# Performance work log

Hardware: AMD Instinct MI355X
Metric: run time of the kernel (lower is better)

## Reference

```python
import jax, jax.numpy as jnp
import numpy as np

B, T, H, W = 32, 100, 16, 16
CIN, HID, COUT, K = 64, 128, 64, 5
EPS = 1e-3      # keras LayerNormalization default epsilon
ALPHA = 0.2     # LeakyReLU slope


def _conv_same(x, w):
    # x: [B,H,W,Cin], w: [kh,kw,Cin,Cout] -> [B,H,W,Cout], SAME padding, stride 1
    return jax.lax.conv_general_dilated(
        x, w, window_strides=(1, 1), padding='SAME',
        dimension_numbers=('NHWC', 'HWIO', 'NHWC'))


def setup_inputs() -> dict:
    key = jax.random.key(0)
    ks = jax.random.split(key, 8)
    s = 0.05
    return {
        'initial_input': jax.random.normal(ks[0], (B, 1, H, W, CIN), jnp.float32),
        'h0': jax.random.normal(ks[1], (B, H, W, HID), jnp.float32) * s,
        'c0': jax.random.normal(ks[2], (B, H, W, HID), jnp.float32) * s,
        'targets': jax.random.normal(ks[3], (B, T, H, W, CIN), jnp.float32),
        'autoreg_prob': jnp.float32(0.5),
        # ConvLSTM2D params (keras gate order: i, f, c, o stacked on last axis)
        'Wx': jax.random.normal(ks[4], (K, K, CIN, 4 * HID), jnp.float32) * s,
        'Wh': jax.random.normal(ks[5], (K, K, HID, 4 * HID), jnp.float32) * s,
        'b': jnp.zeros((4 * HID,), jnp.float32),
        # Conv2D(64, 3, same)
        'conv_w': jax.random.normal(ks[6], (3, 3, HID, COUT), jnp.float32) * s,
        'conv_b': jnp.zeros((COUT,), jnp.float32),
        # LayerNorm (axis=-1)
        'gamma': jnp.ones((COUT,), jnp.float32),
        'beta': jnp.zeros((COUT,), jnp.float32),
    }


def reference(initial_input, h0, c0, targets, autoreg_prob,
              Wx, Wh, b, conv_w, conv_b, gamma, beta):
    T_ = targets.shape[1]
    t_switch = jnp.float32(T_) * autoreg_prob
    x0 = initial_input[:, 0]                       # [B,H,W,CIN] (seq-len-1 ConvLSTM step)
    tgt_t = jnp.transpose(targets, (1, 0, 2, 3, 4))  # [T,B,H,W,CIN]
    ts = jnp.arange(T_)

    def step(carry, inp):
        x, h, c = carry
        t, tgt = inp
        # ConvLSTM2D cell (one timestep)
        g = _conv_same(x, Wx) + _conv_same(h, Wh) + b   # [B,H,W,4*HID]
        i_g, f_g, c_g, o_g = jnp.split(g, 4, axis=-1)
        c = jax.nn.sigmoid(f_g) * c + jax.nn.sigmoid(i_g) * jnp.tanh(c_g)
        h = jax.nn.sigmoid(o_g) * jnp.tanh(c)
        # Conv2D -> LayerNorm(axis=-1) -> LeakyReLU(0.2)
        y = _conv_same(h, conv_w) + conv_b              # [B,H,W,COUT]
        mu = jnp.mean(y, axis=-1, keepdims=True)
        var = jnp.var(y, axis=-1, keepdims=True)
        y = (y - mu) * jax.lax.rsqrt(var + EPS) * gamma + beta
        out = jnp.where(y >= 0, y, ALPHA * y)
        # autoreg phase feeds output back; teacher phase feeds targets[:, t]
        next_x = jnp.where(t.astype(jnp.float32) < t_switch, out, tgt)
        return (next_x, h, c), out

    _, outs = jax.lax.scan(step, (x0, h0, c0), (ts, tgt_t))
    return jnp.transpose(outs, (1, 0, 2, 3, 4))        # [B,T,H,W,COUT]
```

## Files before the change

### kernel.cpp

```cpp
#include <hip/hip_runtime.h>

#define TT   100
#define PADW 20
#define HID  128
#define CIN  64
#define COUT 64
#define ALPHA 0.2f
#define LNEPS 1e-3f

typedef _Float16 f16;
typedef __attribute__((ext_vector_type(8))) _Float16 f16x8;
typedef __attribute__((ext_vector_type(4))) float f32x4;

__device__ __forceinline__ float fsig(float x) {
  return __builtin_amdgcn_rcpf(1.f + __builtin_amdgcn_exp2f(-1.44269504089f * x));
}
__device__ __forceinline__ float ftanh(float x) {
  return 1.f - 2.f * __builtin_amdgcn_rcpf(1.f + __builtin_amdgcn_exp2f(2.88539008178f * x));
}
__device__ __forceinline__ void gload16(const void* g, void* l) {
  __builtin_amdgcn_global_load_lds((const __attribute__((address_space(1))) void*)g,
                                   (__attribute__((address_space(3))) void*)l,
                                   16, 0, 0);
}

__global__ __launch_bounds__(512, 1) void kA6(
    const f16* __restrict__ Xh, const f16* __restrict__ Xl,
    const f16* __restrict__ Hch, const f16* __restrict__ Hcl,
    f16* __restrict__ Hnh, f16* __restrict__ Hnl,
    const f16* __restrict__ Wch, const f16* __restrict__ Wcl,
    const float* __restrict__ bp, float* __restrict__ cst) {
  __shared__ __align__(16) char smem[131072];
  f16 (*sAh)[128][64] = (f16(*)[128][64])(smem);
  f16 (*sAl)[128][64] = (f16(*)[128][64])(smem + 32768);
  f16 (*sBh)[128][64] = (f16(*)[128][64])(smem + 65536);
  f16 (*sBl)[128][64] = (f16(*)[128][64])(smem + 98304);
  float* macc = (float*)smem;

  const int tid = threadIdx.x;
  const int l = tid & 63, w = tid >> 6;
  const int h = w & 1, q = w >> 1;
  const int qm = q >> 1, qn = q & 1;
  const int xcd = blockIdx.x & 7, slot = blockIdx.x >> 3;
  const int ni = xcd >> 1;
  const int mi = ((xcd & 1) << 5) + slot;
  const int cof = ((l & 7) ^ (l >> 3)) * 8;

  int posA[2], wBo[2];
#pragma unroll
  for (int i = 0; i < 2; ++i) {
    const int r = w * 16 + i * 8 + (l >> 3);
    const int m = mi * 128 + r;
    const int b = m >> 8, y = (m >> 4) & 15, x = m & 15;
    posA[i] = (b * PADW + y + 2) * PADW + (x + 2);
    wBo[i] = (ni * 128 + r) * 192 + cof;
  }

  auto stage = [&](int bf, int it) {
    const int tap = it / 3, sub = it - tap * 3;
    const int dy = tap / 5, dx = tap - dy * 5;
    const int dt = (dy - 2) * PADW + (dx - 2);
    if (sub == 0) {
#pragma unroll
      for (int i = 0; i < 2; ++i) {
        gload16(Xh + (posA[i] + dt) * CIN + cof, &sAh[bf][w * 16 + i * 8][0]);
        gload16(Xl + (posA[i] + dt) * CIN + cof, &sAl[bf][w * 16 + i * 8][0]);
      }
    } else {
      const int ho = (sub - 1) * 64 + cof;
#pragma unroll
      for (int i = 0; i < 2; ++i) {
        gload16(Hch + (posA[i] + dt) * HID + ho, &sAh[bf][w * 16 + i * 8][0]);
        gload16(Hcl + (posA[i] + dt) * HID + ho, &sAl[bf][w * 16 + i * 8][0]);
      }
    }
    const int wo = tap * (512 * 192) + sub * 64;
#pragma unroll
    for (int i = 0; i < 2; ++i) {
      gload16(Wch + wBo[i] + wo, &sBh[bf][w * 16 + i * 8][0]);
      gload16(Wcl + wBo[i] + wo, &sBl[bf][w * 16 + i * 8][0]);
    }
  };

  f32x4 acc[4][4] = {};

  stage(0, 0);
  __syncthreads();

  const int co = ((h * 4 + (l >> 4)) ^ (l & 7)) * 8;

  int buf = 0;
  for (int it = 0; it < 75; ++it) {
    if (it < 74) stage(buf ^ 1, it + 1);
    f16x8 avh[4], avl[4], bvh[4], bvl[4];
#pragma unroll
    for (int fm = 0; fm < 4; ++fm) {
      avh[fm] = *(const f16x8*)&sAh[buf][qm * 64 + fm * 16 + (l & 15)][co];
      avl[fm] = *(const f16x8*)&sAl[buf][qm * 64 + fm * 16 + (l & 15)][co];
    }
#pragma unroll
    for (int fn = 0; fn < 4; ++fn) {
      bvh[fn] = *(const f16x8*)&sBh[buf][qn * 64 + fn * 16 + (l & 15)][co];
      bvl[fn] = *(const f16x8*)&sBl[buf][qn * 64 + fn * 16 + (l & 15)][co];
    }
#pragma unroll
    for (int fm = 0; fm < 4; ++fm)
#pragma unroll
      for (int fn = 0; fn < 4; ++fn) {
        acc[fm][fn] =
            __builtin_amdgcn_mfma_f32_16x16x32_f16(avh[fm], bvh[fn], acc[fm][fn], 0, 0, 0);
        acc[fm][fn] =
            __builtin_amdgcn_mfma_f32_16x16x32_f16(avl[fm], bvh[fn], acc[fm][fn], 0, 0, 0);
        acc[fm][fn] =
            __builtin_amdgcn_mfma_f32_16x16x32_f16(avh[fm], bvl[fn], acc[fm][fn], 0, 0, 0);
      }
    __syncthreads();
    buf ^= 1;
  }

  if (h == 1) {
#pragma unroll
    for (int fm = 0; fm < 4; ++fm)
#pragma unroll
      for (int fn = 0; fn < 4; ++fn)
#pragma unroll
        for (int j = 0; j < 4; ++j)
          macc[q * 4096 + ((fm * 4 + fn) * 4 + j) * 64 + l] = acc[fm][fn][j];
  }
  __syncthreads();
  if (h == 0) {
#pragma unroll
    for (int fm = 0; fm < 4; ++fm)
#pragma unroll
      for (int fn = 0; fn < 4; ++fn)
#pragma unroll
        for (int j = 0; j < 4; ++j)
          acc[fm][fn][j] += macc[q * 4096 + ((fm * 4 + fn) * 4 + j) * 64 + l];

#pragma unroll
    for (int fn = 0; fn < 4; ++fn) {
      const int col = ni * 128 + qn * 64 + fn * 16 + (l & 15);
      const float bias = bp[col];
      const int ch = col >> 2;
#pragma unroll
      for (int fm = 0; fm < 4; ++fm) {
#pragma unroll
        for (int j = 0; j < 4; ++j) {
          const float v = acc[fm][fn][j] + bias;
          const float t1 = __shfl_xor(v, 1);
          const float t2 = __shfl_xor(v, 2);
          const float t3 = __shfl_xor(t1, 2);
          if ((l & 3) == 0) {
            const int m = mi * 128 + qm * 64 + fm * 16 + ((l >> 4) << 2) + j;
            const int cidx = m * HID + ch;
            const float cold = cst[cidx];
            const float cn = fsig(t1) * cold + fsig(v) * ftanh(t2);
            cst[cidx] = cn;
            const float hh_ = fsig(t3) * ftanh(cn);
            const int b = m >> 8, y = (m >> 4) & 15, x = m & 15;
            const int pidx = ((b * PADW + y + 2) * PADW + (x + 2)) * HID + ch;
            const f16 hv = (f16)hh_;
            Hnh[pidx] = hv;
            Hnl[pidx] = (f16)(hh_ - (float)hv);
          }
        }
      }
    }
  }
}

__global__ __launch_bounds__(256, 2) void kB(
    const f16* __restrict__ Hnh, const f16* __restrict__ Hnl,
    const f16* __restrict__ Cwh, const f16* __restrict__ Cwl,
    const float* __restrict__ cb, const float* __restrict__ gam,
    const float* __restrict__ bet, const float* __restrict__ tgt,
    const float* __restrict__ prob, float* __restrict__ outp,
    f16* __restrict__ Xph, f16* __restrict__ Xpl, int t) {
  __shared__ __align__(16) f16 sAh[2][32][64];
  __shared__ __align__(16) f16 sAl[2][32][64];
  __shared__ __align__(16) f16 sBh[2][64][64];
  __shared__ __align__(16) f16 sBl[2][64][64];
  __shared__ __align__(16) float yl[32][68];
  const int tid = threadIdx.x;
  const int l = tid & 63, w = tid >> 6;
  const int wm = w >> 1, wn = w & 1;
  const int mi = blockIdx.x;
  const int cof = ((l & 7) ^ (l >> 3)) * 8;

  const int rA = w * 8 + (l >> 3);
  const int mA = mi * 32 + rA;
  const int bA = mA >> 8, yA = (mA >> 4) & 15, xA = mA & 15;
  const int posA = (bA * PADW + yA + 2) * PADW + (xA + 2);
  int wBo[2];
#pragma unroll
  for (int i = 0; i < 2; ++i) wBo[i] = (w * 16 + i * 8 + (l >> 3)) * HID + cof;

  auto stage = [&](int bf, int it) {
    const int tap = it >> 1, sub = it & 1;
    const int dy = tap / 3, dx = tap - dy * 3;
    const int dt = (dy - 1) * PADW + (dx - 1);
    gload16(Hnh + (posA + dt) * HID + sub * 64 + cof, &sAh[bf][w * 8][0]);
    gload16(Hnl + (posA + dt) * HID + sub * 64 + cof, &sAl[bf][w * 8][0]);
    const int wo = tap * (64 * HID) + sub * 64;
#pragma unroll
    for (int i = 0; i < 2; ++i) {
      gload16(Cwh + wBo[i] + wo, &sBh[bf][w * 16 + i * 8][0]);
      gload16(Cwl + wBo[i] + wo, &sBl[bf][w * 16 + i * 8][0]);
    }
  };

  f32x4 acc[2] = {};

  stage(0, 0);
  __syncthreads();

  int buf = 0;
  for (int it = 0; it < 18; ++it) {
    if (it < 17) stage(buf ^ 1, it + 1);
#pragma unroll
    for (int kk = 0; kk < 2; ++kk) {
      const int co = ((kk * 4 + (l >> 4)) ^ (l & 7)) * 8;
      const f16x8 ah = *(const f16x8*)&sAh[buf][wm * 16 + (l & 15)][co];
      const f16x8 al = *(const f16x8*)&sAl[buf][wm * 16 + (l & 15)][co];
#pragma unroll
      for (int fn = 0; fn < 2; ++fn) {
        const f16x8 bh = *(const f16x8*)&sBh[buf][wn * 32 + fn * 16 + (l & 15)][co];
        const f16x8 bl = *(const f16x8*)&sBl[buf][wn * 32 + fn * 16 + (l & 15)][co];
        acc[fn] = __builtin_amdgcn_mfma_f32_16x16x32_f16(ah, bh, acc[fn], 0, 0, 0);
        acc[fn] = __builtin_amdgcn_mfma_f32_16x16x32_f16(al, bh, acc[fn], 0, 0, 0);
        acc[fn] = __builtin_amdgcn_mfma_f32_16x16x32_f16(ah, bl, acc[fn], 0, 0, 0);
      }
    }
    __syncthreads();
    buf ^= 1;
  }

#pragma unroll
  for (int fn = 0; fn < 2; ++fn) {
    const int col = wn * 32 + fn * 16 + (l & 15);
    const float bias = cb[col];
#pragma unroll
    for (int j = 0; j < 4; ++j) yl[wm * 16 + (l >> 4) * 4 + j][col] = acc[fn][j] + bias;
  }
  __syncthreads();

  if (tid < 128) {
    const int row = tid >> 2, part = tid & 3;
    f32x4 vv[4];
    float s = 0.f, q = 0.f;
#pragma unroll
    for (int k2 = 0; k2 < 4; ++k2) {
      vv[k2] = *(const f32x4*)&yl[row][part * 16 + k2 * 4];
#pragma unroll
      for (int e = 0; e < 4; ++e) { const float f = vv[k2][e]; s += f; q += f * f; }
    }
    s += __shfl_xor(s, 1); q += __shfl_xor(q, 1);
    s += __shfl_xor(s, 2); q += __shfl_xor(q, 2);
    const float mean = s * 0.015625f;
    const float var = q * 0.015625f - mean * mean;
    const float rs = __builtin_amdgcn_rsqf(fmaxf(var, 0.f) + LNEPS);
    const int m = mi * 32 + row;
    const int b = m >> 8, pos = m & 255;
    const int py = pos >> 4, px = pos & 15;
    const long obase = (((long)b * TT + t) * 256 + pos) * COUT + part * 16;
    float* op = outp + obase;
    const float* tp = tgt + obase;
    const bool ar = (float)t < 100.f * prob[0];
    const int xoff = ((b * PADW + py + 2) * PADW + px + 2) * CIN + part * 16;
    f16x8 ph[2], pl[2];
#pragma unroll
    for (int k2 = 0; k2 < 4; ++k2) {
      f32x4 o4;
#pragma unroll
      for (int e = 0; e < 4; ++e) {
        const int c = part * 16 + k2 * 4 + e;
        float val = (vv[k2][e] - mean) * rs * gam[c] + bet[c];
        val = val >= 0.f ? val : ALPHA * val;
        o4[e] = val;
        const float nxt = ar ? val : tp[k2 * 4 + e];
        const f16 nh = (f16)nxt;
        const int i16 = k2 * 4 + e;
        ph[i16 >> 3][i16 & 7] = nh;
        pl[i16 >> 3][i16 & 7] = (f16)(nxt - (float)nh);
      }
      *(f32x4*)(op + k2 * 4) = o4;
    }
    *(f16x8*)(Xph + xoff) = ph[0];
    *(f16x8*)(Xph + xoff + 8) = ph[1];
    *(f16x8*)(Xpl + xoff) = pl[0];
    *(f16x8*)(Xpl + xoff + 8) = pl[1];
  }
}

__global__ void k_wcomb(const float* __restrict__ Wx, const float* __restrict__ Wh,
                        f16* __restrict__ Wch, f16* __restrict__ Wcl) {
  const int idx = blockIdx.x * 256 + threadIdx.x;
  if (idx >= 25 * 512 * 192) return;
  const int c = idx % 192, r = idx / 192;
  const int n = r % 512, tap = r / 512;
  const int ch = n >> 2, g = n & 3, no = g * 128 + ch;
  const float v = (c < 64) ? Wx[(tap * 64 + c) * 512 + no]
                           : Wh[(tap * 128 + (c - 64)) * 512 + no];
  const f16 vh = (f16)v;
  Wch[idx] = vh;
  Wcl[idx] = (f16)(v - (float)vh);
}
__global__ void k_wconv(const float* __restrict__ cw, f16* __restrict__ Cwh,
                        f16* __restrict__ Cwl) {
  const int idx = blockIdx.x * 256 + threadIdx.x;
  if (idx >= 9 * 64 * 128) return;
  const int c = idx % 128, r = idx / 128;
  const int n = r % 64, tap = r / 64;
  const float v = cw[(tap * 128 + c) * 64 + n];
  const f16 vh = (f16)v;
  Cwh[idx] = vh;
  Cwl[idx] = (f16)(v - (float)vh);
}
__global__ void k_bperm(const float* __restrict__ b, float* __restrict__ bp) {
  const int n = blockIdx.x * 256 + threadIdx.x;
  if (n < 512) bp[n] = b[(n & 3) * 128 + (n >> 2)];
}
__global__ void k_init(const float* __restrict__ x0, const float* __restrict__ h0,
                       const float* __restrict__ c0, f16* __restrict__ Xph,
                       f16* __restrict__ Xpl, f16* __restrict__ Hh, f16* __restrict__ Hl,
                       float* __restrict__ cst) {
  const int idx = blockIdx.x * 256 + threadIdx.x;
  if (idx < 32 * 256 * 64) {
    const int ch = idx & 63, m = idx >> 6;
    const int b = m >> 8, y = (m >> 4) & 15, x = m & 15;
    const int p = ((b * PADW + y + 2) * PADW + x + 2) * CIN + ch;
    const float v = x0[idx];
    const f16 vh = (f16)v;
    Xph[p] = vh;
    Xpl[p] = (f16)(v - (float)vh);
  } else if (idx < 32 * 256 * 64 + 32 * 256 * 128) {
    const int j = idx - 32 * 256 * 64;
    const int ch = j & 127, m = j >> 7;
    const int b = m >> 8, y = (m >> 4) & 15, x = m & 15;
    const int p = ((b * PADW + y + 2) * PADW + x + 2) * HID + ch;
    const float v = h0[j];
    const f16 vh = (f16)v;
    Hh[p] = vh;
    Hl[p] = (f16)(v - (float)vh);
  } else if (idx < 32 * 256 * 64 + 2 * 32 * 256 * 128) {
    const int j = idx - 32 * 256 * 64 - 32 * 256 * 128;
    cst[j] = c0[j];
  }
}

extern "C" void kernel_launch(void* const* d_in, const int* in_sizes, int n_in,
                              void* d_out, int out_size, void* d_ws, size_t ws_size,
                              hipStream_t stream) {
  (void)in_sizes; (void)n_in; (void)out_size; (void)ws_size;
  const float* x0  = (const float*)d_in[0];
  const float* h0  = (const float*)d_in[1];
  const float* c0  = (const float*)d_in[2];
  const float* tgt = (const float*)d_in[3];
  const float* pr  = (const float*)d_in[4];
  const float* Wx  = (const float*)d_in[5];
  const float* Wh  = (const float*)d_in[6];
  const float* bb  = (const float*)d_in[7];
  const float* cw  = (const float*)d_in[8];
  const float* cbv = (const float*)d_in[9];
  const float* gam = (const float*)d_in[10];
  const float* bet = (const float*)d_in[11];
  float* outp = (float*)d_out;
  char* ws = (char*)d_ws;
  f16*   Xph = (f16*)(ws + 0);
  f16*   Xpl = (f16*)(ws + 1638400);
  f16*   Hh0 = (f16*)(ws + 3276800);
  f16*   Hl0 = (f16*)(ws + 6553600);
  f16*   Hh1 = (f16*)(ws + 9830400);
  f16*   Hl1 = (f16*)(ws + 13107200);
  float* cst = (float*)(ws + 16384000);
  f16*   Wch = (f16*)(ws + 20578304);
  f16*   Wcl = (f16*)(ws + 25493504);
  f16*   Cwh = (f16*)(ws + 30408704);
  f16*   Cwl = (f16*)(ws + 30556160);
  float* bp  = (float*)(ws + 30703616);

  hipMemsetAsync(Xph, 0, 1638400, stream);
  hipMemsetAsync(Xpl, 0, 1638400, stream);
  hipMemsetAsync(Hh0, 0, 3276800, stream);
  hipMemsetAsync(Hl0, 0, 3276800, stream);
  hipMemsetAsync(Hh1, 0, 3276800, stream);
  hipMemsetAsync(Hl1, 0, 3276800, stream);
  k_wcomb<<<9600, 256, 0, stream>>>(Wx, Wh, Wch, Wcl);
  k_wconv<<<288, 256, 0, stream>>>(cw, Cwh, Cwl);
  k_bperm<<<2, 256, 0, stream>>>(bb, bp);
  k_init<<<10240, 256, 0, stream>>>(x0, h0, c0, Xph, Xpl, Hh0, Hl0, cst);

  for (int t = 0; t < TT; ++t) {
    f16* hch = (t & 1) ? Hh1 : Hh0;
    f16* hcl = (t & 1) ? Hl1 : Hl0;
    f16* hnh = (t & 1) ? Hh0 : Hh1;
    f16* hnl = (t & 1) ? Hl0 : Hl1;
    kA6<<<256, 512, 0, stream>>>(Xph, Xpl, hch, hcl, hnh, hnl, Wch, Wcl, bp, cst);
    kB<<<256, 256, 0, stream>>>(hnh, hnl, Cwh, Cwl, cbv, gam, bet, tgt, pr, outp, Xph, Xpl, t);
  }
}
```

Baseline: 13.81 ms.

## Triple-buffer activation tiles and prefetch two stages ahead in ConvLSTM GEMM

The gate-convolution kernel now splits staging into separate activation and weight loads. Activations are triple-buffered and fetched two iterations ahead, while weights stay double-buffered one ahead. A full __syncthreads is replaced by a partial vmcnt wait plus a raw barrier, so the next loads can stay in flight across iterations, and MFMA issue priority is raised with s_setprio. This uses 160KB of LDS and depends on hand-counted vmcnt values, which would be wrong if the compiler issued the loads in a different number or order. The tail iterations redundantly reload stage 74.

```diff
diff --git a/kernel.cpp b/kernel.cpp
--- a/kernel.cpp
+++ b/kernel.cpp
@@ -24,17 +24,17 @@
                                    16, 0, 0);
 }
 
-__global__ __launch_bounds__(512, 1) void kA6(
+__global__ __launch_bounds__(512, 1) void kA7(
     const f16* __restrict__ Xh, const f16* __restrict__ Xl,
     const f16* __restrict__ Hch, const f16* __restrict__ Hcl,
     f16* __restrict__ Hnh, f16* __restrict__ Hnl,
     const f16* __restrict__ Wch, const f16* __restrict__ Wcl,
     const float* __restrict__ bp, float* __restrict__ cst) {
-  __shared__ __align__(16) char smem[131072];
+  __shared__ __align__(16) char smem[163840];
   f16 (*sAh)[128][64] = (f16(*)[128][64])(smem);
-  f16 (*sAl)[128][64] = (f16(*)[128][64])(smem + 32768);
-  f16 (*sBh)[128][64] = (f16(*)[128][64])(smem + 65536);
-  f16 (*sBl)[128][64] = (f16(*)[128][64])(smem + 98304);
+  f16 (*sAl)[128][64] = (f16(*)[128][64])(smem + 49152);
+  f16 (*sBh)[128][64] = (f16(*)[128][64])(smem + 98304);
+  f16 (*sBl)[128][64] = (f16(*)[128][64])(smem + 131072);
   float* macc = (float*)smem;
 
   const int tid = threadIdx.x;
@@ -56,7 +56,7 @@
     wBo[i] = (ni * 128 + r) * 192 + cof;
   }
 
-  auto stage = [&](int bf, int it) {
+  auto stageA = [&](int bf, int it) {
     const int tap = it / 3, sub = it - tap * 3;
     const int dy = tap / 5, dx = tap - dy * 5;
     const int dt = (dy - 2) * PADW + (dx - 2);
@@ -74,6 +74,9 @@
         gload16(Hcl + (posA[i] + dt) * HID + ho, &sAl[bf][w * 16 + i * 8][0]);
       }
     }
+  };
+  auto stageB = [&](int bf, int it) {
+    const int tap = it / 3, sub = it - tap * 3;
     const int wo = tap * (512 * 192) + sub * 64;
 #pragma unroll
     for (int i = 0; i < 2; ++i) {
@@ -84,25 +87,33 @@
 
   f32x4 acc[4][4] = {};
 
-  stage(0, 0);
-  __syncthreads();
+  stageA(0, 0);
+  stageB(0, 0);
+  stageA(1, 1);
+  asm volatile("s_waitcnt vmcnt(4)" ::: "memory");
+  __builtin_amdgcn_s_barrier();
 
   const int co = ((h * 4 + (l >> 4)) ^ (l & 7)) * 8;
 
-  int buf = 0;
-  for (int it = 0; it < 75; ++it) {
-    if (it < 74) stage(buf ^ 1, it + 1);
+  int ca = 0, cb = 0;
+  for (int s = 0; s < 75; ++s) {
+    const int sB = (s + 1 < 75) ? s + 1 : 74;
+    const int sA = (s + 2 < 75) ? s + 2 : 74;
+    stageB(cb ^ 1, sB);
+    int na = ca + 2; if (na >= 3) na -= 3;
+    stageA(na, sA);
     f16x8 avh[4], avl[4], bvh[4], bvl[4];
 #pragma unroll
     for (int fm = 0; fm < 4; ++fm) {
-      avh[fm] = *(const f16x8*)&sAh[buf][qm * 64 + fm * 16 + (l & 15)][co];
-      avl[fm] = *(const f16x8*)&sAl[buf][qm * 64 + fm * 16 + (l & 15)][co];
+      avh[fm] = *(const f16x8*)&sAh[ca][qm * 64 + fm * 16 + (l & 15)][co];
+      avl[fm] = *(const f16x8*)&sAl[ca][qm * 64 + fm * 16 + (l & 15)][co];
     }
 #pragma unroll
     for (int fn = 0; fn < 4; ++fn) {
-      bvh[fn] = *(const f16x8*)&sBh[buf][qn * 64 + fn * 16 + (l & 15)][co];
-      bvl[fn] = *(const f16x8*)&sBl[buf][qn * 64 + fn * 16 + (l & 15)][co];
-    }
+      bvh[fn] = *(const f16x8*)&sBh[cb][qn * 64 + fn * 16 + (l & 15)][co];
+      bvl[fn] = *(const f16x8*)&sBl[cb][qn * 64 + fn * 16 + (l & 15)][co];
+    }
+    __builtin_amdgcn_s_setprio(1);
 #pragma unroll
     for (int fm = 0; fm < 4; ++fm)
 #pragma unroll
@@ -114,9 +125,15 @@
         acc[fm][fn] =
             __builtin_amdgcn_mfma_f32_16x16x32_f16(avh[fm], bvl[fn], acc[fm][fn], 0, 0, 0);
       }
-    __syncthreads();
-    buf ^= 1;
-  }
+    __builtin_amdgcn_s_setprio(0);
+    asm volatile("s_waitcnt vmcnt(4)" ::: "memory");
+    __builtin_amdgcn_s_barrier();
+    ca = (ca == 2) ? 0 : ca + 1;
+    cb ^= 1;
+  }
+
+  asm volatile("s_waitcnt vmcnt(0)" ::: "memory");
+  __builtin_amdgcn_s_barrier();
 
   if (h == 1) {
 #pragma unroll
@@ -395,7 +412,7 @@
     f16* hcl = (t & 1) ? Hl1 : Hl0;
     f16* hnh = (t & 1) ? Hh0 : Hh1;
     f16* hnl = (t & 1) ? Hl0 : Hl1;
-    kA6<<<256, 512, 0, stream>>>(Xph, Xpl, hch, hcl, hnh, hnl, Wch, Wcl, bp, cst);
+    kA7<<<256, 512, 0, stream>>>(Xph, Xpl, hch, hcl, hnh, hnl, Wch, Wcl, bp, cst);
     kB<<<256, 256, 0, stream>>>(hnh, hnl, Cwh, Cwl, cbv, gam, bet, tgt, pr, outp, Xph, Xpl, t);
   }
 }
```

Result: slower. 14.19 ms (+2.7%).

## Stage input halo once per channel chunk and reuse across all 25 conv taps

Applied to the files above, without the earlier changes.

The gate-conv kernel used to reload the A operand (input/hidden pixels) from global memory for every tap and channel chunk. It now loads a 12x20 padded halo tile for each 64-channel chunk into shared memory once and indexes it with per-tap offsets, while only the weights are double-buffered per tap. This cuts A-side global/L2 traffic about 25-fold. The cost is an extra barrier per chunk: the halo load is not overlapped with compute. There may also be LDS bank conflicts from the new swizzled halo indexing.

```diff
diff --git a/kernel.cpp b/kernel.cpp
--- a/kernel.cpp
+++ b/kernel.cpp
@@ -24,17 +24,17 @@
                                    16, 0, 0);
 }
 
-__global__ __launch_bounds__(512, 1) void kA6(
+__global__ __launch_bounds__(512, 1) void kA8(
     const f16* __restrict__ Xh, const f16* __restrict__ Xl,
     const f16* __restrict__ Hch, const f16* __restrict__ Hcl,
     f16* __restrict__ Hnh, f16* __restrict__ Hnl,
     const f16* __restrict__ Wch, const f16* __restrict__ Wcl,
     const float* __restrict__ bp, float* __restrict__ cst) {
-  __shared__ __align__(16) char smem[131072];
-  f16 (*sAh)[128][64] = (f16(*)[128][64])(smem);
-  f16 (*sAl)[128][64] = (f16(*)[128][64])(smem + 32768);
-  f16 (*sBh)[128][64] = (f16(*)[128][64])(smem + 65536);
-  f16 (*sBl)[128][64] = (f16(*)[128][64])(smem + 98304);
+  __shared__ __align__(16) char smem[126976];
+  f16* haloh = (f16*)(smem);
+  f16* halol = (f16*)(smem + 30720);
+  f16 (*sBh)[128][64] = (f16(*)[128][64])(smem + 61440);
+  f16 (*sBl)[128][64] = (f16(*)[128][64])(smem + 94208);
   float* macc = (float*)smem;
 
   const int tid = threadIdx.x;
@@ -44,36 +44,36 @@
   const int xcd = blockIdx.x & 7, slot = blockIdx.x >> 3;
   const int ni = xcd >> 1;
   const int mi = ((xcd & 1) << 5) + slot;
+  const int b_img = mi >> 1;
+  const int ybase = (mi & 1) * 8;
+
   const int cof = ((l & 7) ^ (l >> 3)) * 8;
-
-  int posA[2], wBo[2];
-#pragma unroll
-  for (int i = 0; i < 2; ++i) {
-    const int r = w * 16 + i * 8 + (l >> 3);
-    const int m = mi * 128 + r;
-    const int b = m >> 8, y = (m >> 4) & 15, x = m & 15;
-    posA[i] = (b * PADW + y + 2) * PADW + (x + 2);
-    wBo[i] = (ni * 128 + r) * 192 + cof;
-  }
-
-  auto stage = [&](int bf, int it) {
-    const int tap = it / 3, sub = it - tap * 3;
-    const int dy = tap / 5, dx = tap - dy * 5;
-    const int dt = (dy - 2) * PADW + (dx - 2);
-    if (sub == 0) {
-#pragma unroll
-      for (int i = 0; i < 2; ++i) {
-        gload16(Xh + (posA[i] + dt) * CIN + cof, &sAh[bf][w * 16 + i * 8][0]);
-        gload16(Xl + (posA[i] + dt) * CIN + cof, &sAl[bf][w * 16 + i * 8][0]);
-      }
-    } else {
-      const int ho = (sub - 1) * 64 + cof;
-#pragma unroll
-      for (int i = 0; i < 2; ++i) {
-        gload16(Hch + (posA[i] + dt) * HID + ho, &sAh[bf][w * 16 + i * 8][0]);
-        gload16(Hcl + (posA[i] + dt) * HID + ho, &sAl[bf][w * 16 + i * 8][0]);
-      }
-    }
+  int wBo[2];
+#pragma unroll
+  for (int i = 0; i < 2; ++i) wBo[i] = (ni * 128 + w * 16 + i * 8 + (l >> 3)) * 192 + cof;
+
+  auto stageHalo = [&](int sub) {
+#pragma unroll
+    for (int i2 = 0; i2 < 4; ++i2) {
+      const int gi = w * 4 + i2;
+      if (gi < 30) {
+        const int sabs = gi * 64 + l;
+        const int pix = sabs >> 3, slot3 = sabs & 7;
+        const int hrow = pix / 20, hcol = pix - hrow * 20;
+        const int sc = slot3 ^ (hcol & 7);
+        const int gp = (b_img * PADW + ybase + hrow) * PADW + hcol;
+        if (sub == 0) {
+          gload16(Xh + gp * CIN + sc * 8, haloh + gi * 512);
+          gload16(Xl + gp * CIN + sc * 8, halol + gi * 512);
+        } else {
+          const int ho = (sub - 1) * 64 + sc * 8;
+          gload16(Hch + gp * HID + ho, haloh + gi * 512);
+          gload16(Hcl + gp * HID + ho, halol + gi * 512);
+        }
+      }
+    }
+  };
+  auto stageB = [&](int bf, int tap, int sub) {
     const int wo = tap * (512 * 192) + sub * 64;
 #pragma unroll
     for (int i = 0; i < 2; ++i) {
@@ -84,38 +84,51 @@
 
   f32x4 acc[4][4] = {};
 
-  stage(0, 0);
+  stageHalo(0);
+  stageB(0, 0, 0);
   __syncthreads();
 
-  const int co = ((h * 4 + (l >> 4)) ^ (l & 7)) * 8;
-
-  int buf = 0;
-  for (int it = 0; it < 75; ++it) {
-    if (it < 74) stage(buf ^ 1, it + 1);
-    f16x8 avh[4], avl[4], bvh[4], bvl[4];
-#pragma unroll
-    for (int fm = 0; fm < 4; ++fm) {
-      avh[fm] = *(const f16x8*)&sAh[buf][qm * 64 + fm * 16 + (l & 15)][co];
-      avl[fm] = *(const f16x8*)&sAl[buf][qm * 64 + fm * 16 + (l & 15)][co];
-    }
-#pragma unroll
-    for (int fn = 0; fn < 4; ++fn) {
-      bvh[fn] = *(const f16x8*)&sBh[buf][qn * 64 + fn * 16 + (l & 15)][co];
-      bvl[fn] = *(const f16x8*)&sBl[buf][qn * 64 + fn * 16 + (l & 15)][co];
-    }
-#pragma unroll
-    for (int fm = 0; fm < 4; ++fm)
+  const int kc8 = h * 4 + (l >> 4);
+  const int co = (kc8 ^ (l & 7)) * 8;
+
+  int bufb = 0;
+  for (int sub = 0; sub < 3; ++sub) {
+    if (sub) {
+      stageHalo(sub);
+      __syncthreads();
+    }
+    for (int tap = 0; tap < 25; ++tap) {
+      if (tap + 1 < 25) stageB(bufb ^ 1, tap + 1, sub);
+      else if (sub + 1 < 3) stageB(bufb ^ 1, 0, sub + 1);
+      const int dy = tap / 5, dx = tap - dy * 5;
+      const int hcol = (l & 15) + dx;
+      const int slot3 = kc8 ^ (hcol & 7);
+      const int aoff0 = ((qm * 4 + dy) * 20 + hcol) * 64 + slot3 * 8;
+      f16x8 avh[4], avl[4], bvh[4], bvl[4];
+#pragma unroll
+      for (int fm = 0; fm < 4; ++fm) {
+        avh[fm] = *(const f16x8*)&haloh[aoff0 + fm * 1280];
+        avl[fm] = *(const f16x8*)&halol[aoff0 + fm * 1280];
+      }
 #pragma unroll
       for (int fn = 0; fn < 4; ++fn) {
-        acc[fm][fn] =
-            __builtin_amdgcn_mfma_f32_16x16x32_f16(avh[fm], bvh[fn], acc[fm][fn], 0, 0, 0);
-        acc[fm][fn] =
-            __builtin_amdgcn_mfma_f32_16x16x32_f16(avl[fm], bvh[fn], acc[fm][fn], 0, 0, 0);
-        acc[fm][fn] =
-            __builtin_amdgcn_mfma_f32_16x16x32_f16(avh[fm], bvl[fn], acc[fm][fn], 0, 0, 0);
-      }
-    __syncthreads();
-    buf ^= 1;
+        bvh[fn] = *(const f16x8*)&sBh[bufb][qn * 64 + fn * 16 + (l & 15)][co];
+        bvl[fn] = *(const f16x8*)&sBl[bufb][qn * 64 + fn * 16 + (l & 15)][co];
+      }
+#pragma unroll
+      for (int fm = 0; fm < 4; ++fm)
+#pragma unroll
+        for (int fn = 0; fn < 4; ++fn) {
+          acc[fm][fn] =
+              __builtin_amdgcn_mfma_f32_16x16x32_f16(avh[fm], bvh[fn], acc[fm][fn], 0, 0, 0);
+          acc[fm][fn] =
+              __builtin_amdgcn_mfma_f32_16x16x32_f16(avl[fm], bvh[fn], acc[fm][fn], 0, 0, 0);
+          acc[fm][fn] =
+              __builtin_amdgcn_mfma_f32_16x16x32_f16(avh[fm], bvl[fn], acc[fm][fn], 0, 0, 0);
+        }
+      __syncthreads();
+      bufb ^= 1;
+    }
   }
 
   if (h == 1) {
@@ -395,7 +408,7 @@
     f16* hcl = (t & 1) ? Hl1 : Hl0;
     f16* hnh = (t & 1) ? Hh0 : Hh1;
     f16* hnl = (t & 1) ? Hl0 : Hl1;
-    kA6<<<256, 512, 0, stream>>>(Xph, Xpl, hch, hcl, hnh, hnl, Wch, Wcl, bp, cst);
+    kA8<<<256, 512, 0, stream>>>(Xph, Xpl, hch, hcl, hnh, hnl, Wch, Wcl, bp, cst);
     kB<<<256, 256, 0, stream>>>(hnh, hnl, Cwh, Cwl, cbv, gam, bet, tgt, pr, outp, Xph, Xpl, t);
   }
 }
```

Result: faster. 12.72 ms, median of 3 (-7.9%).
